# Optimization experiments

Measured on AMD Instinct MI355X. Metric: run time of the kernel, lower is better.

## Reference

```python
import jax, jax.numpy as jnp
import numpy as np

B, H, L, D = 4, 8, 2048, 64
FACTOR = 5


def setup_inputs() -> dict:
    key = jax.random.key(0)
    kq, kk, kv, ki = jax.random.split(key, 4)
    sample_k = min(FACTOR * int(np.ceil(np.log(L))), L)  # = 40
    queries = jax.random.normal(kq, (B, H, L, D), jnp.float32)
    keys = jax.random.normal(kk, (B, H, L, D), jnp.float32)
    values = jax.random.normal(kv, (B, H, L, D), jnp.float32)
    index_sample = jax.random.randint(ki, (L, sample_k), 0, L)
    return {"queries": queries, "keys": keys, "values": values,
            "index_sample": index_sample}


def prob_attention(queries, keys, values, index_sample):
    Bq, Hq, L_Q, Dk = queries.shape
    L_K = keys.shape[2]
    n_top = min(FACTOR * int(np.ceil(np.log(L_Q))), L_Q)  # u
    scale = float(1.0 / np.sqrt(Dk))

    # --- _prob_QK: sample scores for each query over random key subset ---
    # K_sample: (B,H,L_Q,S,D); index_sample shared across batch/heads
    K_sample = keys[:, :, index_sample, :]
    Q_K_sample = jnp.einsum('bhld,bhlsd->bhls', queries, K_sample)
    # sparsity measure M = max - mean (mean over full L_K as in source)
    M = Q_K_sample.max(-1) - Q_K_sample.sum(-1) / L_K      # (B,H,L_Q)
    M_top = jax.lax.top_k(M, n_top)[1]                     # (B,H,u) query indices

    # full scores only for the selected "active" queries
    Q_reduce = jnp.take_along_axis(queries, M_top[..., None], axis=2)  # (B,H,u,D)
    scores = jnp.einsum('bhud,bhkd->bhuk', Q_reduce, keys) * scale     # (B,H,u,L_K)

    # --- causal ProbMask: key j masked when j > selected query position ---
    causal = jnp.arange(L_K)[None, None, None, :] > M_top[..., None]
    scores = jnp.where(causal, -jnp.inf, scores)
    attn = jax.nn.softmax(scores, axis=-1)
    ctx_update = jnp.einsum('bhuk,bhkd->bhud', attn, values)           # (B,H,u,D)

    # --- initial context (causal branch): running cumulative sum of V ---
    context = jnp.cumsum(values, axis=2)                               # (B,H,L_Q,D)

    # scatter active-query results back into the context
    b_idx = jnp.arange(Bq)[:, None, None]
    h_idx = jnp.arange(Hq)[None, :, None]
    context = context.at[b_idx, h_idx, M_top].set(ctx_update)
    return context


def reference(queries, keys, values, index_sample):
    return prob_attention(queries, keys, values, index_sample)
```

## Files before the change

kernel.cpp:

```cpp
#include <hip/hip_runtime.h>
#include <hip/hip_bf16.h>
#include <cstdint>

#define BB 4
#define HH 8
#define LL 2048
#define DD 64
#define SK 40
#define NT 40
#define BHN (BB*HH)
#define SCALE 0.125f
#define CHUNK 128
#define NCH (LL/CHUNK)
#define USPL 2
#define UPB (NT/USPL)

#define WS_M    0
#define WS_SUB  (WS_M + BHN*LL)
#define WS_CTX  (WS_SUB + BHN*64*DD)
#define WS_PM   (WS_CTX + BHN*NT*DD)
#define WS_PSUM (WS_PM + BHN*NT*NCH)
#define WS_PACC (WS_PSUM + BHN*NT*NCH)
#define WS_TOP  (WS_PACC + BHN*NT*NCH*DD)

#define K1_BLOCKS (BHN * LL / 4)
#define K4A_BLOCKS (BHN * 64)
#define K4B_BLOCKS (BHN * 64)

static __device__ __forceinline__ float4 f4add(float4 a, float4 b) {
    float4 r; r.x = a.x + b.x; r.y = a.y + b.y; r.z = a.z + b.z; r.w = a.w + b.w; return r;
}

__global__ __launch_bounds__(256) void f1_m_sub(const float* __restrict__ Q,
                                                const float* __restrict__ K,
                                                const int* __restrict__ isamp,
                                                const float* __restrict__ V,
                                                float* __restrict__ M,
                                                float* __restrict__ sub) {
    int bid = blockIdx.x;
    if (bid < K1_BLOCKS) {
        int swz  = (bid & 7) * (K1_BLOCKS / 8) + (bid >> 3);
        int wid  = swz * 4 + (threadIdx.x >> 6);
        int lane = threadIdx.x & 63;
        int bh   = wid >> 11;
        int l    = wid & (LL - 1);
        int g    = lane >> 4;
        int e    = lane & 15;

        float4 q = reinterpret_cast<const float4*>(Q + (size_t)wid * DD)[e];
        const float* Kbh = K + (size_t)bh * LL * DD;
        const int* irow = isamp + l * SK;

        int idxs[SK / 4];
#pragma unroll
        for (int p = 0; p < SK / 4; p++) idxs[p] = irow[p * 4 + g];

        float mx = -INFINITY, sm = 0.f;
#pragma unroll
        for (int b = 0; b < 2; b++) {
            float4 kv[5];
#pragma unroll
            for (int i = 0; i < 5; i++)
                kv[i] = reinterpret_cast<const float4*>(Kbh + (size_t)idxs[b * 5 + i] * DD)[e];
            float dd[5];
#pragma unroll
            for (int i = 0; i < 5; i++)
                dd[i] = q.x * kv[i].x + q.y * kv[i].y + q.z * kv[i].z + q.w * kv[i].w;
#pragma unroll
            for (int i = 0; i < 5; i++) {
                float d = dd[i];
                d += __shfl_xor(d, 1);
                d += __shfl_xor(d, 2);
                d += __shfl_xor(d, 4);
                d += __shfl_xor(d, 8);
                mx = fmaxf(mx, d);
                sm += d;
            }
        }
        mx = fmaxf(mx, __shfl_xor(mx, 16));
        mx = fmaxf(mx, __shfl_xor(mx, 32));
        sm += __shfl_xor(sm, 16);
        sm += __shfl_xor(sm, 32);
        if (lane == 0) M[wid] = mx - sm * (1.0f / (float)LL);
    } else {
        __shared__ float4 part[16][16];
        int blk = bid - K1_BLOCKS;
        int t = threadIdx.x;
        int d4 = t & 15, rg = t >> 4;
        const float4* v4 = reinterpret_cast<const float4*>(V) + (size_t)blk * 32 * 16 + (size_t)rg * 2 * 16 + d4;
        float4 a = v4[0], b = v4[16];
        part[rg][d4] = f4add(a, b);
        __syncthreads();
#pragma unroll
        for (int step = 8; step; step >>= 1) {
            if (rg < step) part[rg][d4] = f4add(part[rg][d4], part[rg + step][d4]);
            __syncthreads();
        }
        if (rg == 0)
            reinterpret_cast<float4*>(sub)[(size_t)blk * 16 + d4] = part[0][d4];
    }
}

__global__ __launch_bounds__(256) void f2_topk_scan(const float* __restrict__ M,
                                                    int* __restrict__ Mtop,
                                                    const float* __restrict__ V,
                                                    const float* __restrict__ sub,
                                                    float* __restrict__ out) {
    int bid = blockIdx.x;
    if (bid < BHN) {
        int lane = threadIdx.x;
        if (lane >= 64) return;
        int bh = bid;
        const float* Mb = M + (size_t)bh * LL;
        unsigned long long key[32];
#pragma unroll
        for (int j = 0; j < 32; j++) {
            int i = lane + j * 64;
            unsigned u = __float_as_uint(Mb[i]);
            u = (u & 0x80000000u) ? ~u : (u | 0x80000000u);
            key[j] = ((unsigned long long)u << 32) | (unsigned)(~i);
        }
        unsigned long long winner = 0ull;
        for (int t = 0; t < NT; t++) {
            unsigned long long best = 0ull;
#pragma unroll
            for (int j = 0; j < 32; j++) {
                unsigned long long k = key[j];
                k = (k == winner) ? 0ull : k;
                key[j] = k;
                best = (k > best) ? k : best;
            }
#pragma unroll
            for (int off = 32; off; off >>= 1) {
                unsigned long long o = __shfl_xor(best, off);
                best = (o > best) ? o : best;
            }
            winner = best;
            if (lane == 0) Mtop[bh * NT + t] = (int)(~(unsigned)(best & 0xFFFFFFFFull));
        }
    } else {
        __shared__ float4 plds[16][16];
        int blk = bid - BHN;
        int bh = blk >> 6, j = blk & 63;
        int t = threadIdx.x;
        int d4 = t & 15, rg = t >> 4;

        const float4* sub4 = reinterpret_cast<const float4*>(sub) + (size_t)(bh * 64) * 16 + d4;
        float4 off = {0.f, 0.f, 0.f, 0.f};
        for (int p = 0; p < j; p++) off = f4add(off, sub4[(size_t)p * 16]);

        const float4* v4 = reinterpret_cast<const float4*>(V) + (size_t)blk * 32 * 16 + (size_t)rg * 2 * 16 + d4;
        float4 a = v4[0], b = v4[16];
        plds[rg][d4] = f4add(a, b);
        __syncthreads();
        float4 ex = {0.f, 0.f, 0.f, 0.f};
        for (int p = 0; p < rg; p++) ex = f4add(ex, plds[p][d4]);

        float4 r0 = f4add(f4add(off, ex), a);
        float4 r1 = f4add(r0, b);
        float4* o4 = reinterpret_cast<float4*>(out) + (size_t)blk * 32 * 16 + (size_t)rg * 2 * 16 + d4;
        o4[0] = r0;
        o4[16] = r1;
    }
}

__global__ __launch_bounds__(256) void k3a_partial(const float* __restrict__ Q,
                                                   const float* __restrict__ K,
                                                   const float* __restrict__ V,
                                                   const int* __restrict__ Mtop,
                                                   float* __restrict__ pm,
                                                   float* __restrict__ psum,
                                                   float* __restrict__ pacc) {
    __shared__ float q_lds[UPB * DD];
    __shared__ float s_lds[UPB][CHUNK];
    __shared__ int   qi_lds[UPB];
    int bid = blockIdx.x;
    int swz = (bid & 7) * (BHN * NCH * USPL / 8) + (bid >> 3);
    int bh  = swz >> 5;
    int rem = swz & 31;
    int ch  = rem >> 1;
    int u0  = (rem & 1) * UPB;
    int ck  = ch * CHUNK;
    int tid = threadIdx.x;

    if (tid < UPB) qi_lds[tid] = Mtop[bh * NT + u0 + tid];
    __syncthreads();
    for (int c = tid; c < UPB * 16; c += 256) {
        int u = c >> 4, j = c & 15;
        reinterpret_cast<float4*>(q_lds)[c] =
            reinterpret_cast<const float4*>(Q + ((size_t)bh * LL + qi_lds[u]) * DD)[j];
    }
    __syncthreads();

    int k    = ck + (tid >> 1);
    int half = tid & 1;
    const float4* krow = reinterpret_cast<const float4*>(K + ((size_t)bh * LL + k) * DD) + half * 8;
    float4 kreg[8];
#pragma unroll
    for (int j = 0; j < 8; j++) kreg[j] = krow[j];
#pragma unroll 4
    for (int u = 0; u < UPB; u++) {
        const float4* q4 = reinterpret_cast<const float4*>(q_lds + u * DD) + half * 8;
        float d = 0.f;
#pragma unroll
        for (int j = 0; j < 8; j++) {
            float4 a = q4[j], b = kreg[j];
            d += a.x * b.x + a.y * b.y + a.z * b.z + a.w * b.w;
        }
        d += __shfl_xor(d, 1);
        float s = (k <= qi_lds[u]) ? d * SCALE : -INFINITY;
        if (half == 0) s_lds[u][k - ck] = s;
    }
    __syncthreads();

    int w = tid >> 6, lane = tid & 63;
#pragma unroll
    for (int uu = 0; uu < UPB / 4; uu++) {
        int u = w + uu * 4;
        float s0 = s_lds[u][lane], s1 = s_lds[u][lane + 64];
        float m = fmaxf(s0, s1);
#pragma unroll
        for (int off = 32; off; off >>= 1) m = fmaxf(m, __shfl_xor(m, off));
        float e0 = (s0 == -INFINITY) ? 0.f : __expf(s0 - m);
        float e1 = (s1 == -INFINITY) ? 0.f : __expf(s1 - m);
        s_lds[u][lane] = e0;
        s_lds[u][lane + 64] = e1;
        float smv = e0 + e1;
#pragma unroll
        for (int off = 32; off; off >>= 1) smv += __shfl_xor(smv, off);
        if (lane == 0) {
            size_t rg = (size_t)bh * NT + u0 + u;
            pm  [rg * NCH + ch] = m;
            psum[rg * NCH + ch] = smv;
        }
    }
    __syncthreads();

    int d4 = lane & 15, kp = lane >> 4;
    float4 acc[UPB / 4];
#pragma unroll
    for (int uu = 0; uu < UPB / 4; uu++) acc[uu] = make_float4(0.f, 0.f, 0.f, 0.f);
    const float4* v4 = reinterpret_cast<const float4*>(V + ((size_t)bh * LL + ck) * DD) + d4;
#pragma unroll 4
    for (int kb = 0; kb < CHUNK; kb += 4) {
        int kk = kb + kp;
        float4 v = v4[(size_t)kk * 16];
#pragma unroll
        for (int uu = 0; uu < UPB / 4; uu++) {
            float s = s_lds[w + uu * 4][kk];
            acc[uu].x += s * v.x;
            acc[uu].y += s * v.y;
            acc[uu].z += s * v.z;
            acc[uu].w += s * v.w;
        }
    }
#pragma unroll
    for (int uu = 0; uu < UPB / 4; uu++) {
        float4 a = acc[uu];
        a.x += __shfl_xor(a.x, 16); a.x += __shfl_xor(a.x, 32);
        a.y += __shfl_xor(a.y, 16); a.y += __shfl_xor(a.y, 32);
        a.z += __shfl_xor(a.z, 16); a.z += __shfl_xor(a.z, 32);
        a.w += __shfl_xor(a.w, 16); a.w += __shfl_xor(a.w, 32);
        if (kp == 0) {
            size_t rg = (size_t)bh * NT + u0 + w + uu * 4;
            reinterpret_cast<float4*>(pacc + (rg * NCH + ch) * DD)[d4] = a;
        }
    }
}

__global__ __launch_bounds__(64) void k3b_scatter(const float* __restrict__ pm,
                                                  const float* __restrict__ psum,
                                                  const float* __restrict__ pacc,
                                                  const int* __restrict__ Mtop,
                                                  float* __restrict__ out) {
    int row = blockIdx.x;
    int lane = threadIdx.x;
    int bh = row / NT;
    float pmv[NCH];
    float m = -INFINITY;
#pragma unroll
    for (int i = 0; i < NCH; i++) {
        pmv[i] = pm[(size_t)row * NCH + i];
        m = fmaxf(m, pmv[i]);
    }
    float Z = 0.f, acc = 0.f;
#pragma unroll
    for (int i = 0; i < NCH; i++) {
        float sc = (pmv[i] == -INFINITY) ? 0.f : __expf(pmv[i] - m);
        Z   += psum[(size_t)row * NCH + i] * sc;
        acc += pacc[((size_t)row * NCH + i) * DD + lane] * sc;
    }
    int qi = Mtop[row];
    out[((size_t)bh * LL + qi) * DD + lane] = acc / Z;
}

extern "C" void kernel_launch(void* const* d_in, const int* in_sizes, int n_in,
                              void* d_out, int out_size, void* d_ws, size_t ws_size,
                              hipStream_t stream) {
    const float* Q = (const float*)d_in[0];
    const float* K = (const float*)d_in[1];
    const float* V = (const float*)d_in[2];
    const int* isamp = (const int*)d_in[3];
    float* ws   = (float*)d_ws;
    float* M    = ws + WS_M;
    float* sub  = ws + WS_SUB;
    float* pm   = ws + WS_PM;
    float* psum = ws + WS_PSUM;
    float* pacc = ws + WS_PACC;
    int*   Mtop = (int*)(ws + WS_TOP);
    float* out  = (float*)d_out;

    f1_m_sub    <<<K1_BLOCKS + K4A_BLOCKS, 256, 0, stream>>>(Q, K, isamp, V, M, sub);
    f2_topk_scan<<<BHN + K4B_BLOCKS,       256, 0, stream>>>(M, Mtop, V, sub, out);
    k3a_partial <<<BHN * NCH * USPL,       256, 0, stream>>>(Q, K, V, Mtop, pm, psum, pacc);
    k3b_scatter <<<BHN * NT,                64, 0, stream>>>(pm, psum, pacc, Mtop, out);
}
```

Baseline: 176.9 us.

## Bucket sampled key indices by chunk and stage K chunks in LDS

A new preprocessing pass groups each query's 40 sampled key indices by which 256-row key chunk they fall in, storing byte-sized row offsets and per-chunk boundaries. A new kernel loads each key chunk into LDS once per block and computes partial max and sum of sampled scores per chunk, replacing random global gathers of K rows. The top-k kernel then merges the eight partials to form M. This adds a kernel launch, partial-result traffic, and divergent variable-length loops over the bucketed samples.

```diff
diff --git a/kernel.cpp b/kernel.cpp
--- a/kernel.cpp
+++ b/kernel.cpp
@@ -15,6 +15,10 @@
 #define USPL 2
 #define UPB (NT/USPL)
 
+#define KC 8
+#define KCR (LL/KC)
+#define KPAD 68
+
 #define WS_M    0
 #define WS_SUB  (WS_M + BHN*LL)
 #define WS_CTX  (WS_SUB + BHN*64*DD)
@@ -23,68 +27,44 @@
 #define WS_PACC (WS_PSUM + BHN*NT*NCH)
 #define WS_TOP  (WS_PACC + BHN*NT*NCH*DD)
 
-#define K1_BLOCKS (BHN * LL / 4)
 #define K4A_BLOCKS (BHN * 64)
 #define K4B_BLOCKS (BHN * 64)
+#define PRE_BLOCKS (LL / 256)
 
 static __device__ __forceinline__ float4 f4add(float4 a, float4 b) {
     float4 r; r.x = a.x + b.x; r.y = a.y + b.y; r.z = a.z + b.z; r.w = a.w + b.w; return r;
 }
 
-__global__ __launch_bounds__(256) void f1_m_sub(const float* __restrict__ Q,
-                                                const float* __restrict__ K,
-                                                const int* __restrict__ isamp,
-                                                const float* __restrict__ V,
-                                                float* __restrict__ M,
-                                                float* __restrict__ sub) {
+__global__ __launch_bounds__(256) void f0_pre_sub(const int* __restrict__ isamp,
+                                                  const float* __restrict__ V,
+                                                  unsigned char* __restrict__ rows8,
+                                                  unsigned long long* __restrict__ off8,
+                                                  float* __restrict__ sub) {
     int bid = blockIdx.x;
-    if (bid < K1_BLOCKS) {
-        int swz  = (bid & 7) * (K1_BLOCKS / 8) + (bid >> 3);
-        int wid  = swz * 4 + (threadIdx.x >> 6);
-        int lane = threadIdx.x & 63;
-        int bh   = wid >> 11;
-        int l    = wid & (LL - 1);
-        int g    = lane >> 4;
-        int e    = lane & 15;
-
-        float4 q = reinterpret_cast<const float4*>(Q + (size_t)wid * DD)[e];
-        const float* Kbh = K + (size_t)bh * LL * DD;
-        const int* irow = isamp + l * SK;
-
-        int idxs[SK / 4];
-#pragma unroll
-        for (int p = 0; p < SK / 4; p++) idxs[p] = irow[p * 4 + g];
-
-        float mx = -INFINITY, sm = 0.f;
-#pragma unroll
-        for (int b = 0; b < 2; b++) {
-            float4 kv[5];
-#pragma unroll
-            for (int i = 0; i < 5; i++)
-                kv[i] = reinterpret_cast<const float4*>(Kbh + (size_t)idxs[b * 5 + i] * DD)[e];
-            float dd[5];
-#pragma unroll
-            for (int i = 0; i < 5; i++)
-                dd[i] = q.x * kv[i].x + q.y * kv[i].y + q.z * kv[i].z + q.w * kv[i].w;
-#pragma unroll
-            for (int i = 0; i < 5; i++) {
-                float d = dd[i];
-                d += __shfl_xor(d, 1);
-                d += __shfl_xor(d, 2);
-                d += __shfl_xor(d, 4);
-                d += __shfl_xor(d, 8);
-                mx = fmaxf(mx, d);
-                sm += d;
+    if (bid < PRE_BLOCKS) {
+        int l = bid * 256 + threadIdx.x;
+        int idxr[SK];
+#pragma unroll
+        for (int s = 0; s < SK; s++) idxr[s] = isamp[l * SK + s];
+        unsigned long long off = 0ull;
+        int end = 0;
+#pragma unroll
+        for (int c = 0; c < KC; c++) {
+            int p = end;
+#pragma unroll
+            for (int s = 0; s < SK; s++) {
+                if ((idxr[s] >> 8) == c) {
+                    rows8[l * SK + p] = (unsigned char)(idxr[s] & 255);
+                    p++;
+                }
             }
-        }
-        mx = fmaxf(mx, __shfl_xor(mx, 16));
-        mx = fmaxf(mx, __shfl_xor(mx, 32));
-        sm += __shfl_xor(sm, 16);
-        sm += __shfl_xor(sm, 32);
-        if (lane == 0) M[wid] = mx - sm * (1.0f / (float)LL);
+            end = p;
+            off |= (unsigned long long)end << (6 * c);
+        }
+        off8[l] = off;
     } else {
         __shared__ float4 part[16][16];
-        int blk = bid - K1_BLOCKS;
+        int blk = bid - PRE_BLOCKS;
         int t = threadIdx.x;
         int d4 = t & 15, rg = t >> 4;
         const float4* v4 = reinterpret_cast<const float4*>(V) + (size_t)blk * 32 * 16 + (size_t)rg * 2 * 16 + d4;
@@ -101,7 +81,59 @@
     }
 }
 
-__global__ __launch_bounds__(256) void f2_topk_scan(const float* __restrict__ M,
+__global__ __launch_bounds__(256) void k1_chunk(const float* __restrict__ Q,
+                                                const float* __restrict__ K,
+                                                const unsigned char* __restrict__ rows8,
+                                                const unsigned long long* __restrict__ off8,
+                                                float* __restrict__ pmax8,
+                                                float* __restrict__ psum8) {
+    extern __shared__ float K_lds[];
+    int bid = blockIdx.x;
+    int x = bid & 7;
+    int kslot = bid >> 3;
+    int g = x * 32 + (kslot & 31);
+    int lhalf = kslot >> 5;
+    int bh = g >> 3, c = g & 7;
+    int tid = threadIdx.x;
+
+    const float4* Ksrc = reinterpret_cast<const float4*>(K + ((size_t)bh * LL + c * KCR) * DD);
+#pragma unroll
+    for (int i = tid; i < KCR * 16; i += 256) {
+        int row = i >> 4, e = i & 15;
+        *reinterpret_cast<float4*>(&K_lds[row * KPAD + e * 4]) = Ksrc[i];
+    }
+    __syncthreads();
+
+    int w = tid >> 6, lane = tid & 63;
+    int g4 = lane >> 4, e = lane & 15;
+    for (int iter = 0; iter < 64; iter++) {
+        int l = lhalf * 1024 + iter * 16 + w * 4 + g4;
+        unsigned long long off = off8[l];
+        int start = c ? (int)((off >> (6 * (c - 1))) & 63) : 0;
+        int end   = (int)((off >> (6 * c)) & 63);
+        float4 q = *reinterpret_cast<const float4*>(Q + ((size_t)bh * LL + l) * DD + e * 4);
+        float mx = -INFINITY, sm = 0.f;
+        for (int j = start; j < end; j++) {
+            int r = rows8[l * SK + j];
+            float4 kv = *reinterpret_cast<const float4*>(&K_lds[r * KPAD + e * 4]);
+            float d = q.x * kv.x + q.y * kv.y + q.z * kv.z + q.w * kv.w;
+            d += __shfl_xor(d, 1);
+            d += __shfl_xor(d, 2);
+            d += __shfl_xor(d, 4);
+            d += __shfl_xor(d, 8);
+            mx = fmaxf(mx, d);
+            sm += d;
+        }
+        if (e == 0) {
+            size_t o = ((size_t)c * BHN + bh) * LL + l;
+            pmax8[o] = mx;
+            psum8[o] = sm;
+        }
+    }
+}
+
+__global__ __launch_bounds__(256) void f2_topk_scan(const float* __restrict__ pmax8,
+                                                    const float* __restrict__ psum8,
                                                     int* __restrict__ Mtop,
                                                     const float* __restrict__ V,
                                                     const float* __restrict__ sub,
@@ -111,12 +143,19 @@
         int lane = threadIdx.x;
         if (lane >= 64) return;
         int bh = bid;
-        const float* Mb = M + (size_t)bh * LL;
         unsigned long long key[32];
 #pragma unroll
         for (int j = 0; j < 32; j++) {
             int i = lane + j * 64;
-            unsigned u = __float_as_uint(Mb[i]);
+            float mx = -INFINITY, sm = 0.f;
+#pragma unroll
+            for (int c = 0; c < KC; c++) {
+                size_t o = ((size_t)c * BHN + bh) * LL + i;
+                mx = fmaxf(mx, pmax8[o]);
+                sm += psum8[o];
+            }
+            float v = mx - sm * (1.0f / (float)LL);
+            unsigned u = __float_as_uint(v);
             u = (u & 0x80000000u) ? ~u : (u | 0x80000000u);
             key[j] = ((unsigned long long)u << 32) | (unsigned)(~i);
         }
@@ -302,7 +341,6 @@
     const float* V = (const float*)d_in[2];
     const int* isamp = (const int*)d_in[3];
     float* ws   = (float*)d_ws;
-    float* M    = ws + WS_M;
     float* sub  = ws + WS_SUB;
     float* pm   = ws + WS_PM;
     float* psum = ws + WS_PSUM;
@@ -310,8 +348,14 @@
     int*   Mtop = (int*)(ws + WS_TOP);
     float* out  = (float*)d_out;
 
-    f1_m_sub    <<<K1_BLOCKS + K4A_BLOCKS, 256, 0, stream>>>(Q, K, isamp, V, M, sub);
-    f2_topk_scan<<<BHN + K4B_BLOCKS,       256, 0, stream>>>(M, Mtop, V, sub, out);
-    k3a_partial <<<BHN * NCH * USPL,       256, 0, stream>>>(Q, K, V, Mtop, pm, psum, pacc);
-    k3b_scatter <<<BHN * NT,                64, 0, stream>>>(pm, psum, pacc, Mtop, out);
-}
+    unsigned char* rows8 = (unsigned char*)(ws + WS_CTX);
+    unsigned long long* off8 = (unsigned long long*)(ws + WS_CTX + 20480);
+    float* pmax8 = pacc;
+    float* psum8 = pacc + (size_t)KC * BHN * LL;
+
+    f0_pre_sub <<<PRE_BLOCKS + K4A_BLOCKS, 256, 0, stream>>>(isamp, V, rows8, off8, sub);
+    k1_chunk   <<<BHN * KC * 2, 256, KCR * KPAD * 4, stream>>>(Q, K, rows8, off8, pmax8, psum8);
+    f2_topk_scan<<<BHN + K4B_BLOCKS, 256, 0, stream>>>(pmax8, psum8, Mtop, V, sub, out);
+    k3a_partial<<<BHN * NCH * USPL, 256, 0, stream>>>(Q, K, V, Mtop, pm, psum, pacc);
+    k3b_scatter<<<BHN * NT, 64, 0, stream>>>(pm, psum, pacc, Mtop, out);
+}
```

New measurement: 359.1 us. +103.0%, slower.
